# Kernel optimization log

Hardware: AMD Instinct MI355X
Metric: run time of the kernel (lower is better)

Reference implementation:

```python
import jax, jax.numpy as jnp
import numpy as np
import math

B, S, D, H = 2, 2048, 1024, 16
DH = D // H
MASK_VALUE = -1e6


def setup_inputs() -> dict:
    key = jax.random.key(0)
    ks = jax.random.split(key, 6)
    x = jax.random.normal(ks[0], (B, S, D), dtype=jnp.float32)
    scale = 1.0 / math.sqrt(D)
    Wq = jax.random.normal(ks[1], (D, D), dtype=jnp.float32) * scale
    Wk = jax.random.normal(ks[2], (D, D), dtype=jnp.float32) * scale
    Wv = jax.random.normal(ks[3], (D, D), dtype=jnp.float32) * scale
    Wo = jax.random.normal(ks[4], (D, D), dtype=jnp.float32) * scale
    valid_lens = jax.random.randint(ks[5], (B,), 1, S + 1, dtype=jnp.int32)
    return {"x": x, "Wq": Wq, "Wk": Wk, "Wv": Wv, "Wo": Wo, "valid_lens": valid_lens}


def reference(x, Wq, Wk, Wv, Wo, valid_lens):
    # Projections (Linear with bias=False): [B,S,D] -> split into H heads of DH
    def split_heads(y):
        return y.reshape(B, S, H, DH).transpose(0, 2, 1, 3)  # [B,H,S,DH]

    q = split_heads(x @ Wq)
    k = split_heads(x @ Wk)
    v = split_heads(x @ Wv)

    # scores [B,H,Sq,Sk]; masking depends only on key position per batch
    scores = jnp.einsum("bhqd,bhkd->bhqk", q, k) / math.sqrt(DH)
    key_pos = jnp.arange(S, dtype=jnp.int32)  # [Sk]
    mask = key_pos[None, None, None, :] < valid_lens[:, None, None, None]
    scores = jnp.where(mask, scores, MASK_VALUE)
    attn = jax.nn.softmax(scores, axis=-1)  # dropout is identity in eval

    out = jnp.einsum("bhqk,bhkd->bhqd", attn, v)  # [B,H,S,DH]
    out = out.transpose(0, 2, 1, 3).reshape(B, S, D)  # concat heads
    return out @ Wo
```

## Files before the change

### kernel.cpp

```cpp
#include <hip/hip_runtime.h>

#define Bdim 2
#define Sdim 2048
#define Ddim 1024
#define Hdim 16

typedef unsigned short u16;
typedef u16 u16x8 __attribute__((ext_vector_type(8)));
typedef u16 u16x4 __attribute__((ext_vector_type(4)));
typedef unsigned u32x4 __attribute__((ext_vector_type(4)));
typedef __bf16 bf16x8 __attribute__((ext_vector_type(8)));
typedef float f32x4 __attribute__((ext_vector_type(4)));
typedef float f32x16 __attribute__((ext_vector_type(16)));

static __device__ __forceinline__ u16 f2bf(float f) {
  unsigned u = __float_as_uint(f);
  u += 0x7fffu + ((u >> 16) & 1u);
  return (u16)(u >> 16);
}
static __device__ __forceinline__ float bf2f(u16 v) {
  return __uint_as_float((unsigned)v << 16);
}
static __device__ __forceinline__ bf16x8 asbf(u16x8 v) {
  return __builtin_bit_cast(bf16x8, v);
}
static __device__ __forceinline__ f32x4 mfma16(bf16x8 a, bf16x8 b, f32x4 c) {
  return __builtin_amdgcn_mfma_f32_16x16x32_bf16(a, b, c, 0, 0, 0);
}
static __device__ __forceinline__ f32x16 mfma32(bf16x8 a, bf16x8 b, f32x16 c) {
  return __builtin_amdgcn_mfma_f32_32x32x16_bf16(a, b, c, 0, 0, 0);
}

__global__ __launch_bounds__(256) void cvtx(const float* __restrict__ x,
                                            u16* __restrict__ xb) {
  int i = blockIdx.x * 256 + threadIdx.x;
  const float4* xp = (const float4*)x;
  float4 a = xp[2 * i], b = xp[2 * i + 1];
  u16x8 o;
  o[0] = f2bf(a.x); o[1] = f2bf(a.y); o[2] = f2bf(a.z); o[3] = f2bf(a.w);
  o[4] = f2bf(b.x); o[5] = f2bf(b.y); o[6] = f2bf(b.z); o[7] = f2bf(b.w);
  ((u16x8*)xb)[i] = o;
}

__global__ __launch_bounds__(256) void transw(
    const float* __restrict__ W0, const float* __restrict__ W1,
    const float* __restrict__ W2, const float* __restrict__ W3,
    u16* __restrict__ T0, u16* __restrict__ T1,
    u16* __restrict__ T2, u16* __restrict__ T3) {
  const float* W = blockIdx.z == 0 ? W0 : blockIdx.z == 1 ? W1 : blockIdx.z == 2 ? W2 : W3;
  u16* T = blockIdx.z == 0 ? T0 : blockIdx.z == 1 ? T1 : blockIdx.z == 2 ? T2 : T3;
  __shared__ float tile[32][33];
  const int t = threadIdx.x;
  const int k0 = blockIdx.x * 32, n0 = blockIdx.y * 32;
  const int r = t >> 3, cq = (t & 7) * 4;
  float4 v = *(const float4*)(W + (size_t)(k0 + r) * Ddim + n0 + cq);
  tile[r][cq] = v.x; tile[r][cq + 1] = v.y; tile[r][cq + 2] = v.z; tile[r][cq + 3] = v.w;
  __syncthreads();
  u16x4 ov;
  ov[0] = f2bf(tile[cq][r]);
  ov[1] = f2bf(tile[cq + 1][r]);
  ov[2] = f2bf(tile[cq + 2][r]);
  ov[3] = f2bf(tile[cq + 3][r]);
  *(u16x4*)(T + (size_t)(n0 + r) * Ddim + k0 + cq) = ov;
}

__global__ __launch_bounds__(256) void vtrans(const u16* __restrict__ V,
                                              u16* __restrict__ Vt) {
  __shared__ u16 tile[32][72];
  const int t = threadIdx.x;
  const int s0 = blockIdx.x * 32;
  const int bh = blockIdx.y, b = bh >> 4, h = bh & 15;
  {
    int sl = t >> 3, dq = (t & 7) * 8;
    u16x8 v = *(const u16x8*)(V + (size_t)(b * Sdim + s0 + sl) * Ddim + h * 64 + dq);
    *(u16x8*)(&tile[sl][dq]) = v;
  }
  __syncthreads();
  {
    int dl = t >> 2, sq = (t & 3) * 8;
    u16x8 v;
#pragma unroll
    for (int i = 0; i < 8; i++) v[i] = tile[sq + i][dl];
    int s = s0 + sq;
    int kt = s >> 6, c = (s >> 3) & 7;
    *(u16x8*)(Vt + ((((size_t)bh * 32 + kt) * 8 + c) * 64 + dl) * 8) = v;
  }
}

__global__ __launch_bounds__(256) void tilek(const u16* __restrict__ K,
                                             u16* __restrict__ Kt) {
  int tid = blockIdx.x * 256 + threadIdx.x;
  int row = tid & 63;
  int c = (tid >> 6) & 7;
  int kt = (tid >> 9) & 31;
  int bh = tid >> 14;
  int b = bh >> 4, h = bh & 15;
  u16x8 kc = *(const u16x8*)(K + (size_t)(b * Sdim + kt * 64 + row) * Ddim + h * 64 + c * 8);
  ((u16x8*)Kt)[tid] = kc;
}

template <bool F32OUT>
__global__ __launch_bounds__(256) void gemm128(
    const u16* __restrict__ A,
    const u16* __restrict__ Bt0, const u16* __restrict__ Bt1, const u16* __restrict__ Bt2,
    void* __restrict__ C0v, void* __restrict__ C1v, void* __restrict__ C2v) {
  __shared__ u16 As[128 * 64];
  __shared__ u16 Bs[128 * 64];
  const int zz = blockIdx.y >> 3;
  const u16* Bt = (zz == 0) ? Bt0 : (zz == 1) ? Bt1 : Bt2;
  void* Cv = (zz == 0) ? C0v : (zz == 1) ? C1v : C2v;

  const int t = threadIdx.x;
  const int lane = t & 63, w = t >> 6;
  const int wm = w >> 1, wn = w & 1;
  const int c = lane & 15, g = lane >> 4;
  const int m0 = blockIdx.x * 128, n0 = (blockIdx.y & 7) * 128;
  const float oscale = (!F32OUT && zz == 0) ? 0.125f : 1.0f;

  const f32x4 zv = {0.f, 0.f, 0.f, 0.f};
  f32x4 acc[4][4];
#pragma unroll
  for (int m = 0; m < 4; m++)
#pragma unroll
    for (int n = 0; n < 4; n++) acc[m][n] = zv;

  u16x8 ra[4], rb[4];
#pragma unroll
  for (int i = 0; i < 4; i++) {
    int idx = t + 256 * i;
    int row = idx >> 3, ch = idx & 7;
    ra[i] = *(const u16x8*)(A + (size_t)(m0 + row) * 1024 + ch * 8);
    rb[i] = *(const u16x8*)(Bt + (size_t)(n0 + row) * 1024 + ch * 8);
  }
#pragma unroll
  for (int i = 0; i < 4; i++) {
    int idx = t + 256 * i;
    int row = idx >> 3, ch = idx & 7;
    int sw = (ch ^ (row & 7)) * 8;
    *(u16x8*)(As + row * 64 + sw) = ra[i];
    *(u16x8*)(Bs + row * 64 + sw) = rb[i];
  }
  __syncthreads();

  for (int kt = 0; kt < 1024; kt += 64) {
    const bool more = (kt + 64) < 1024;
    if (more) {
#pragma unroll
      for (int i = 0; i < 4; i++) {
        int idx = t + 256 * i;
        int row = idx >> 3, ch = idx & 7;
        ra[i] = *(const u16x8*)(A + (size_t)(m0 + row) * 1024 + kt + 64 + ch * 8);
        rb[i] = *(const u16x8*)(Bt + (size_t)(n0 + row) * 1024 + kt + 64 + ch * 8);
      }
    }
#pragma unroll
    for (int kh = 0; kh < 2; kh++) {
      bf16x8 af[4], bfr[4];
#pragma unroll
      for (int m = 0; m < 4; m++) {
        int row = wm * 64 + m * 16 + c;
        int chr = kh * 4 + g;
        af[m] = asbf(*(const u16x8*)(As + row * 64 + ((chr ^ (row & 7)) * 8)));
      }
#pragma unroll
      for (int n = 0; n < 4; n++) {
        int row = wn * 64 + n * 16 + c;
        int chr = kh * 4 + g;
        bfr[n] = asbf(*(const u16x8*)(Bs + row * 64 + ((chr ^ (row & 7)) * 8)));
      }
#pragma unroll
      for (int m = 0; m < 4; m++)
#pragma unroll
        for (int n = 0; n < 4; n++) acc[m][n] = mfma16(af[m], bfr[n], acc[m][n]);
    }
    if (more) {
      __syncthreads();
#pragma unroll
      for (int i = 0; i < 4; i++) {
        int idx = t + 256 * i;
        int row = idx >> 3, ch = idx & 7;
        int sw = (ch ^ (row & 7)) * 8;
        *(u16x8*)(As + row * 64 + sw) = ra[i];
        *(u16x8*)(Bs + row * 64 + sw) = rb[i];
      }
      __syncthreads();
    }
  }
#pragma unroll
  for (int m = 0; m < 4; m++)
#pragma unroll
    for (int n = 0; n < 4; n++)
#pragma unroll
      for (int r = 0; r < 4; r++) {
        int row = m0 + wm * 64 + m * 16 + 4 * g + r;
        int col = n0 + wn * 64 + n * 16 + c;
        if (F32OUT)
          ((float*)Cv)[(size_t)row * 1024 + col] = acc[m][n][r];
        else
          ((u16*)Cv)[(size_t)row * 1024 + col] = f2bf(acc[m][n][r] * oscale);
      }
}

__global__ __launch_bounds__(64, 4) void attn_kernel(
    const u16* __restrict__ Q, const u16* __restrict__ Kt,
    const u16* __restrict__ Vt, const int* __restrict__ vlen,
    u16* __restrict__ O, u16* __restrict__ Opart, float2* __restrict__ mlp) {
  __shared__ u16 ot[32][72];
  const int lane = threadIdx.x;
  const int q = lane & 31, hi = lane >> 5;
  const int bh = blockIdx.y, b = bh >> 4, h = bh & 15;
  const int q0 = blockIdx.x * 32;
  const int nv = vlen[b];
  const int NS = gridDim.z, z = blockIdx.z;

  bf16x8 qf[4];
  {
    const u16* qp = Q + (size_t)(b * Sdim + q0 + q) * Ddim + h * 64 + hi * 8;
#pragma unroll
    for (int s = 0; s < 4; s++) qf[s] = asbf(*(const u16x8*)(qp + s * 16));
  }

  f32x16 o0, o1;
#pragma unroll
  for (int r = 0; r < 16; r++) { o0[r] = 0.f; o1[r] = 0.f; }
  float m = -3.0e38f, l = 0.f;

  const int nt = (nv + 63) >> 6;
  const int chunk = (nt + NS - 1) / NS;
  const int t0 = z * chunk;
  const int t1 = min(nt, t0 + chunk);
  for (int kt = t0; kt < t1; ++kt) {
    const int k0 = kt * 64;
    const u16* Ktile = Kt + ((size_t)bh * 32 + kt) * 4096;
    const u16* Vtile = Vt + ((size_t)bh * 32 + kt) * 4096;
    f32x16 sc[2];
#pragma unroll
    for (int kb = 0; kb < 2; kb++) {
      f32x16 acc;
#pragma unroll
      for (int r = 0; r < 16; r++) acc[r] = 0.f;
#pragma unroll
      for (int s = 0; s < 4; s++) {
        bf16x8 kf = asbf(*(const u16x8*)(Ktile + (2 * s + hi) * 512 + (kb * 32 + q) * 8));
        acc = mfma32(kf, qf[s], acc);
      }
      sc[kb] = acc;
    }
    if (k0 + 64 > nv) {
#pragma unroll
      for (int kb = 0; kb < 2; kb++)
#pragma unroll
        for (int r = 0; r < 16; r++) {
          int key = k0 + kb * 32 + (r & 3) + 8 * (r >> 2) + 4 * hi;
          if (key >= nv) sc[kb][r] = -1e30f;
        }
    }
    float mx[16];
#pragma unroll
    for (int r = 0; r < 16; r++) mx[r] = fmaxf(sc[0][r], sc[1][r]);
#pragma unroll
    for (int st = 8; st > 0; st >>= 1)
#pragma unroll
      for (int r = 0; r < st; r++) mx[r] = fmaxf(mx[r], mx[r + st]);
    float tm = fmaxf(mx[0], __shfl_xor(mx[0], 32));
    if (!__all(tm <= m + 8.f)) {
      float mn = fmaxf(m, tm);
      float al = __expf(m - mn);
#pragma unroll
      for (int r = 0; r < 16; r++) { o0[r] *= al; o1[r] *= al; }
      l *= al;
      m = mn;
    }
    unsigned pw[4][4];
    float s0 = 0.f, s1 = 0.f, s2 = 0.f, s3 = 0.f;
#pragma unroll
    for (int kb = 0; kb < 2; kb++)
#pragma unroll
      for (int hh = 0; hh < 2; hh++)
#pragma unroll
        for (int wi = 0; wi < 4; wi++) {
          float e0 = __expf(sc[kb][hh * 8 + wi * 2] - m);
          float e1 = __expf(sc[kb][hh * 8 + wi * 2 + 1] - m);
          if (wi == 0) s0 += e0 + e1;
          else if (wi == 1) s1 += e0 + e1;
          else if (wi == 2) s2 += e0 + e1;
          else s3 += e0 + e1;
          asm("v_cvt_pk_bf16_f32 %0, %1, %2"
              : "=v"(pw[kb * 2 + hh][wi]) : "v"(e0), "v"(e1));
        }
    float ssum = (s0 + s1) + (s2 + s3);
    ssum += __shfl_xor(ssum, 32);
    l += ssum;
#pragma unroll
    for (int f = 0; f < 4; f++) {
      asm("v_permlane32_swap_b32 %0, %1" : "+v"(pw[f][0]), "+v"(pw[f][2]));
      asm("v_permlane32_swap_b32 %0, %1" : "+v"(pw[f][1]), "+v"(pw[f][3]));
    }
#pragma unroll
    for (int f = 0; f < 4; f++) {
      u32x4 wv = {pw[f][0], pw[f][1], pw[f][2], pw[f][3]};
      bf16x8 pa = __builtin_bit_cast(bf16x8, wv);
      bf16x8 va = asbf(*(const u16x8*)(Vtile + (2 * f + hi) * 512 + q * 8));
      bf16x8 vb = asbf(*(const u16x8*)(Vtile + (2 * f + hi) * 512 + (32 + q) * 8));
      o0 = mfma32(va, pa, o0);
      o1 = mfma32(vb, pa, o1);
    }
  }
  const float scale = (NS == 1) ? (1.f / l) : 1.f;
#pragma unroll
  for (int r = 0; r < 16; r++) {
    const int dh = (r & 3) + 8 * (r >> 2) + 4 * hi;
    ot[q][dh] = f2bf(o0[r] * scale);
    ot[q][32 + dh] = f2bf(o1[r] * scale);
  }
  asm volatile("s_waitcnt lgkmcnt(0)" ::: "memory");
  __builtin_amdgcn_sched_barrier(0);
  if (NS == 1) {
    u16* op = O + (size_t)(b * Sdim + q0 + q) * Ddim + h * 64 + hi * 32;
#pragma unroll
    for (int j = 0; j < 4; j++)
      *(u16x8*)(op + j * 8) = *(const u16x8*)(&ot[q][hi * 32 + j * 8]);
  } else {
    u16* op = Opart + ((size_t)(z * 32 + bh) * Sdim + q0 + q) * 64 + hi * 32;
#pragma unroll
    for (int j = 0; j < 4; j++)
      *(u16x8*)(op + j * 8) = *(const u16x8*)(&ot[q][hi * 32 + j * 8]);
    if (hi == 0)
      mlp[(size_t)(z * 32 + bh) * Sdim + q0 + q] = make_float2(m, l);
  }
}

template <int NS>
__global__ __launch_bounds__(256) void attn_combine(
    const u16* __restrict__ Opart, const float2* __restrict__ mlp,
    u16* __restrict__ O) {
  const int t = threadIdx.x;
  const int bh = blockIdx.y, b = bh >> 4, h = bh & 15;
  const int q = blockIdx.x * 32 + (t >> 3);
  const int d0 = (t & 7) * 8;
  float2 ml[NS];
  float M = -3.0e38f;
#pragma unroll
  for (int z = 0; z < NS; z++) {
    ml[z] = mlp[(size_t)(z * 32 + bh) * Sdim + q];
    M = fmaxf(M, ml[z].x);
  }
  float acc[8];
#pragma unroll
  for (int i = 0; i < 8; i++) acc[i] = 0.f;
  float wsum = 0.f;
#pragma unroll
  for (int z = 0; z < NS; z++) {
    float w = __expf(ml[z].x - M);
    wsum += w * ml[z].y;
    u16x8 ov = *(const u16x8*)(Opart + ((size_t)(z * 32 + bh) * Sdim + q) * 64 + d0);
#pragma unroll
    for (int i = 0; i < 8; i++) acc[i] += w * bf2f(ov[i]);
  }
  const float inv = 1.f / wsum;
  u16x8 res;
#pragma unroll
  for (int i = 0; i < 8; i++) res[i] = f2bf(acc[i] * inv);
  *(u16x8*)(O + ((size_t)b * Sdim + q) * Ddim + h * 64 + d0) = res;
}

extern "C" void kernel_launch(void* const* d_in, const int* in_sizes, int n_in,
                              void* d_out, int out_size, void* d_ws, size_t ws_size,
                              hipStream_t stream) {
  const float* x = (const float*)d_in[0];
  const float* Wq = (const float*)d_in[1];
  const float* Wk = (const float*)d_in[2];
  const float* Wv = (const float*)d_in[3];
  const float* Wo = (const float*)d_in[4];
  const int* vl = (const int*)d_in[5];
  float* out = (float*)d_out;

  char* ws = (char*)d_ws;
  const size_t SZ_X = (size_t)Bdim * Sdim * Ddim * sizeof(u16);
  const size_t SZ_W = (size_t)Ddim * Ddim * sizeof(u16);
  u16* xb = (u16*)ws; ws += SZ_X;
  u16* WqT = (u16*)ws; ws += SZ_W;
  u16* WkT = (u16*)ws; ws += SZ_W;
  u16* WvT = (u16*)ws; ws += SZ_W;
  u16* WoT = (u16*)ws; ws += SZ_W;
  u16* Qb = (u16*)ws; ws += SZ_X;
  u16* Kb = (u16*)ws; ws += SZ_X;
  u16* Vb = (u16*)ws; ws += SZ_X;
  u16* Ob = (u16*)ws; ws += SZ_X;
  u16* Ktb = (u16*)ws; ws += SZ_X;
  u16* Vtb = (u16*)ws; ws += SZ_X;

  const size_t PER_SPLIT = (size_t)Bdim * Hdim * Sdim * 64 * sizeof(u16) +
                           (size_t)Bdim * Hdim * Sdim * sizeof(float2);
  size_t used = (size_t)(ws - (char*)d_ws);
  size_t avail = (ws_size > used) ? ws_size - used : 0;
  int NS = (avail >= 4 * PER_SPLIT) ? 4 : (avail >= 2 * PER_SPLIT) ? 2 : 1;
  u16* Opart = (u16*)ws;
  float2* mlp = (float2*)(ws + (size_t)NS * Bdim * Hdim * Sdim * 64 * sizeof(u16));

  cvtx<<<dim3((Bdim * Sdim * Ddim) / (8 * 256)), 256, 0, stream>>>(x, xb);
  transw<<<dim3(32, 32, 4), 256, 0, stream>>>(Wq, Wk, Wv, Wo, WqT, WkT, WvT, WoT);
  gemm128<false><<<dim3(32, 24), 256, 0, stream>>>(xb, WqT, WkT, WvT, Qb, Kb, Vb);
  vtrans<<<dim3(Sdim / 32, Bdim * Hdim), 256, 0, stream>>>(Vb, Vtb);
  tilek<<<dim3((Bdim * Sdim * Ddim / 8) / 256), 256, 0, stream>>>(Kb, Ktb);
  attn_kernel<<<dim3(Sdim / 32, Bdim * Hdim, NS), 64, 0, stream>>>(Qb, Ktb, Vtb, vl, Ob,
                                                                   Opart, mlp);
  if (NS == 4)
    attn_combine<4><<<dim3(Sdim / 32, Bdim * Hdim), 256, 0, stream>>>(Opart, mlp, Ob);
  else if (NS == 2)
    attn_combine<2><<<dim3(Sdim / 32, Bdim * Hdim), 256, 0, stream>>>(Opart, mlp, Ob);
  gemm128<true><<<dim3(32, 8), 256, 0, stream>>>(Ob, WoT, WoT, WoT, out, out, out);
}
```

Baseline: 126.6 us.

## Store GEMM operands in pre-tiled 128x64 cell layout for contiguous tile loads

Introduces a tiled storage layout in which each 128-row by 64-column bf16 tile is one contiguous 16 KB block. The x conversion, weight transpose, attention output and combine kernels all write in this layout. Both GEMMs then fetch each K-step tile as a single linear run of 16-byte vectors instead of 128 strided row segments, aiming for better coalescing and fewer DRAM pages touched. The producer kernels' stores become more scattered in exchange.

```diff
diff --git a/kernel.cpp b/kernel.cpp
--- a/kernel.cpp
+++ b/kernel.cpp
@@ -31,15 +31,20 @@
   return __builtin_amdgcn_mfma_f32_32x32x16_bf16(a, b, c, 0, 0, 0);
 }
 
+static __device__ __forceinline__ size_t tcell(int R, int k) {
+  return ((size_t)(R >> 7) * 16 + (k >> 6)) * 1024 + (R & 127) * 8 + ((k >> 3) & 7);
+}
+
 __global__ __launch_bounds__(256) void cvtx(const float* __restrict__ x,
-                                            u16* __restrict__ xb) {
+                                            u16* __restrict__ xt) {
   int i = blockIdx.x * 256 + threadIdx.x;
   const float4* xp = (const float4*)x;
   float4 a = xp[2 * i], b = xp[2 * i + 1];
   u16x8 o;
   o[0] = f2bf(a.x); o[1] = f2bf(a.y); o[2] = f2bf(a.z); o[3] = f2bf(a.w);
   o[4] = f2bf(b.x); o[5] = f2bf(b.y); o[6] = f2bf(b.z); o[7] = f2bf(b.w);
-  ((u16x8*)xb)[i] = o;
+  int R = i >> 7, k = (i & 127) * 8;
+  ((u16x8*)xt)[tcell(R, k)] = o;
 }
 
 __global__ __launch_bounds__(256) void transw(
@@ -61,7 +66,8 @@
   ov[1] = f2bf(tile[cq + 1][r]);
   ov[2] = f2bf(tile[cq + 2][r]);
   ov[3] = f2bf(tile[cq + 3][r]);
-  *(u16x4*)(T + (size_t)(n0 + r) * Ddim + k0 + cq) = ov;
+  int n = n0 + r, k = k0 + cq;
+  *(u16x4*)(T + tcell(n, k) * 8 + (k & 7)) = ov;
 }
 
 __global__ __launch_bounds__(256) void vtrans(const u16* __restrict__ V,
@@ -114,7 +120,7 @@
   const int lane = t & 63, w = t >> 6;
   const int wm = w >> 1, wn = w & 1;
   const int c = lane & 15, g = lane >> 4;
-  const int m0 = blockIdx.x * 128, n0 = (blockIdx.y & 7) * 128;
+  const int mb = blockIdx.x, nb = blockIdx.y & 7;
   const float oscale = (!F32OUT && zz == 0) ? 0.125f : 1.0f;
 
   const f32x4 zv = {0.f, 0.f, 0.f, 0.f};
@@ -124,13 +130,13 @@
 #pragma unroll
     for (int n = 0; n < 4; n++) acc[m][n] = zv;
 
+  const u16x8* Ac = (const u16x8*)A;
+  const u16x8* Bc = (const u16x8*)Bt;
   u16x8 ra[4], rb[4];
 #pragma unroll
   for (int i = 0; i < 4; i++) {
-    int idx = t + 256 * i;
-    int row = idx >> 3, ch = idx & 7;
-    ra[i] = *(const u16x8*)(A + (size_t)(m0 + row) * 1024 + ch * 8);
-    rb[i] = *(const u16x8*)(Bt + (size_t)(n0 + row) * 1024 + ch * 8);
+    ra[i] = Ac[(size_t)(mb * 16 + 0) * 1024 + t + 256 * i];
+    rb[i] = Bc[(size_t)(nb * 16 + 0) * 1024 + t + 256 * i];
   }
 #pragma unroll
   for (int i = 0; i < 4; i++) {
@@ -142,15 +148,13 @@
   }
   __syncthreads();
 
-  for (int kt = 0; kt < 1024; kt += 64) {
-    const bool more = (kt + 64) < 1024;
+  for (int kt = 0; kt < 16; ++kt) {
+    const bool more = (kt + 1) < 16;
     if (more) {
 #pragma unroll
       for (int i = 0; i < 4; i++) {
-        int idx = t + 256 * i;
-        int row = idx >> 3, ch = idx & 7;
-        ra[i] = *(const u16x8*)(A + (size_t)(m0 + row) * 1024 + kt + 64 + ch * 8);
-        rb[i] = *(const u16x8*)(Bt + (size_t)(n0 + row) * 1024 + kt + 64 + ch * 8);
+        ra[i] = Ac[(size_t)(mb * 16 + kt + 1) * 1024 + t + 256 * i];
+        rb[i] = Bc[(size_t)(nb * 16 + kt + 1) * 1024 + t + 256 * i];
       }
     }
 #pragma unroll
@@ -192,8 +196,8 @@
     for (int n = 0; n < 4; n++)
 #pragma unroll
       for (int r = 0; r < 4; r++) {
-        int row = m0 + wm * 64 + m * 16 + 4 * g + r;
-        int col = n0 + wn * 64 + n * 16 + c;
+        int row = mb * 128 + wm * 64 + m * 16 + 4 * g + r;
+        int col = nb * 128 + wn * 64 + n * 16 + c;
         if (F32OUT)
           ((float*)Cv)[(size_t)row * 1024 + col] = acc[m][n][r];
         else
@@ -316,10 +320,11 @@
   asm volatile("s_waitcnt lgkmcnt(0)" ::: "memory");
   __builtin_amdgcn_sched_barrier(0);
   if (NS == 1) {
-    u16* op = O + (size_t)(b * Sdim + q0 + q) * Ddim + h * 64 + hi * 32;
+    int R = b * Sdim + q0 + q;
+    size_t cellbase = ((size_t)(R >> 7) * 16 + h) * 1024 + (R & 127) * 8 + hi * 4;
 #pragma unroll
     for (int j = 0; j < 4; j++)
-      *(u16x8*)(op + j * 8) = *(const u16x8*)(&ot[q][hi * 32 + j * 8]);
+      ((u16x8*)O)[cellbase + j] = *(const u16x8*)(&ot[q][hi * 32 + j * 8]);
   } else {
     u16* op = Opart + ((size_t)(z * 32 + bh) * Sdim + q0 + q) * 64 + hi * 32;
 #pragma unroll
@@ -361,7 +366,8 @@
   u16x8 res;
 #pragma unroll
   for (int i = 0; i < 8; i++) res[i] = f2bf(acc[i] * inv);
-  *(u16x8*)(O + ((size_t)b * Sdim + q) * Ddim + h * 64 + d0) = res;
+  int R = b * Sdim + q;
+  ((u16x8*)O)[((size_t)(R >> 7) * 16 + h) * 1024 + (R & 127) * 8 + (d0 >> 3)] = res;
 }
 
 extern "C" void kernel_launch(void* const* d_in, const int* in_sizes, int n_in,
@@ -378,7 +384,7 @@
   char* ws = (char*)d_ws;
   const size_t SZ_X = (size_t)Bdim * Sdim * Ddim * sizeof(u16);
   const size_t SZ_W = (size_t)Ddim * Ddim * sizeof(u16);
-  u16* xb = (u16*)ws; ws += SZ_X;
+  u16* xt = (u16*)ws; ws += SZ_X;
   u16* WqT = (u16*)ws; ws += SZ_W;
   u16* WkT = (u16*)ws; ws += SZ_W;
   u16* WvT = (u16*)ws; ws += SZ_W;
@@ -386,7 +392,7 @@
   u16* Qb = (u16*)ws; ws += SZ_X;
   u16* Kb = (u16*)ws; ws += SZ_X;
   u16* Vb = (u16*)ws; ws += SZ_X;
-  u16* Ob = (u16*)ws; ws += SZ_X;
+  u16* Obt = (u16*)ws; ws += SZ_X;
   u16* Ktb = (u16*)ws; ws += SZ_X;
   u16* Vtb = (u16*)ws; ws += SZ_X;
 
@@ -398,16 +404,16 @@
   u16* Opart = (u16*)ws;
   float2* mlp = (float2*)(ws + (size_t)NS * Bdim * Hdim * Sdim * 64 * sizeof(u16));
 
-  cvtx<<<dim3((Bdim * Sdim * Ddim) / (8 * 256)), 256, 0, stream>>>(x, xb);
+  cvtx<<<dim3((Bdim * Sdim * Ddim) / (8 * 256)), 256, 0, stream>>>(x, xt);
   transw<<<dim3(32, 32, 4), 256, 0, stream>>>(Wq, Wk, Wv, Wo, WqT, WkT, WvT, WoT);
-  gemm128<false><<<dim3(32, 24), 256, 0, stream>>>(xb, WqT, WkT, WvT, Qb, Kb, Vb);
+  gemm128<false><<<dim3(32, 24), 256, 0, stream>>>(xt, WqT, WkT, WvT, Qb, Kb, Vb);
   vtrans<<<dim3(Sdim / 32, Bdim * Hdim), 256, 0, stream>>>(Vb, Vtb);
   tilek<<<dim3((Bdim * Sdim * Ddim / 8) / 256), 256, 0, stream>>>(Kb, Ktb);
-  attn_kernel<<<dim3(Sdim / 32, Bdim * Hdim, NS), 64, 0, stream>>>(Qb, Ktb, Vtb, vl, Ob,
+  attn_kernel<<<dim3(Sdim / 32, Bdim * Hdim, NS), 64, 0, stream>>>(Qb, Ktb, Vtb, vl, Obt,
                                                                    Opart, mlp);
   if (NS == 4)
-    attn_combine<4><<<dim3(Sdim / 32, Bdim * Hdim), 256, 0, stream>>>(Opart, mlp, Ob);
+    attn_combine<4><<<dim3(Sdim / 32, Bdim * Hdim), 256, 0, stream>>>(Opart, mlp, Obt);
   else if (NS == 2)
-    attn_combine<2><<<dim3(Sdim / 32, Bdim * Hdim), 256, 0, stream>>>(Opart, mlp, Ob);
-  gemm128<true><<<dim3(32, 8), 256, 0, stream>>>(Ob, WoT, WoT, WoT, out, out, out);
-}
+    attn_combine<2><<<dim3(Sdim / 32, Bdim * Hdim), 256, 0, stream>>>(Opart, mlp, Obt);
+  gemm128<true><<<dim3(32, 8), 256, 0, stream>>>(Obt, WoT, WoT, WoT, out, out, out);
+}
```

Result: faster. 121.5 us (-4.0%).
